# Kernel tuning notes

Hardware: AMD Instinct MI355X
Metric: run time of the kernel (lower is better)

Reference implementation:

```python
import jax, jax.numpy as jnp
import numpy as np

D_MODEL = 1024
D_INNER = 2048   # expand_factor * d_model
D_STATE = 16
D_CONV = 4
DT_RANK = 64     # ceil(d_model / 16)
EPS = 1e-5


def setup_inputs() -> dict:
    key = jax.random.key(0)
    ks = jax.random.split(key, 10)
    B, L = 2, 1024
    w = lambda k, shape, s: (jax.random.normal(k, shape, jnp.float32) * s)
    A = jnp.tile(jnp.arange(1, D_STATE + 1, dtype=jnp.float32), (D_INNER, 1))
    return {
        "hidden_states": jax.random.normal(ks[0], (B, L, D_MODEL), jnp.float32),
        "norm_w": jnp.ones((D_MODEL,), jnp.float32),
        "norm_b": jnp.zeros((D_MODEL,), jnp.float32),
        "in_proj_w": w(ks[1], (D_MODEL, 2 * D_INNER), 0.02),
        "conv_w": w(ks[2], (D_INNER, D_CONV), 0.2),
        "conv_b": jnp.zeros((D_INNER,), jnp.float32),
        "x_proj_w": w(ks[3], (D_INNER, DT_RANK + 2 * D_STATE), 0.02),
        "dt_proj_w": w(ks[4], (DT_RANK, D_INNER), 0.1),
        "dt_proj_b": w(ks[5], (D_INNER,), 0.1),
        "A_log": jnp.log(A),
        "D_param": jnp.ones((D_INNER,), jnp.float32),
        "out_proj_w": w(ks[6], (D_INNER, D_MODEL), 0.02),
    }


def _causal_depthwise_conv(x, conv_w, conv_b):
    # x: [B, L, d_inner] -> causal depthwise conv, kernel size D_CONV
    B, L, C = x.shape
    xt = jnp.transpose(x, (0, 2, 1))                 # [B, C, L]
    xt = jnp.pad(xt, ((0, 0), (0, 0), (D_CONV - 1, 0)))  # left pad == torch pad+truncate
    k = conv_w[:, None, :]                            # [C, 1, K] (OIH, groups=C)
    y = jax.lax.conv_general_dilated(
        xt, k, window_strides=(1,), padding="VALID",
        dimension_numbers=("NCH", "OIH", "NCH"), feature_group_count=C)
    y = y + conv_b[None, :, None]
    return jnp.transpose(y, (0, 2, 1))                # [B, L, C]


def _selective_scan(u, delta, A, Bm, Cm, D_param):
    # u, delta: [B, L, d_inner]; A: [d_inner, d_state]; Bm, Cm: [B, L, d_state]
    dA = jnp.exp(delta[..., None] * A[None, None])            # [B,L,d,n]
    dBu = delta[..., None] * Bm[:, :, None, :] * u[..., None]  # [B,L,d,n]
    h0 = jnp.zeros((u.shape[0], u.shape[2], A.shape[1]), u.dtype)

    def step(h, inp):
        dA_t, dBu_t, c_t = inp          # [B,d,n], [B,d,n], [B,n]
        h = dA_t * h + dBu_t
        y = jnp.einsum("bdn,bn->bd", h, c_t)
        return h, y

    xs = (jnp.moveaxis(dA, 1, 0), jnp.moveaxis(dBu, 1, 0), jnp.moveaxis(Cm, 1, 0))
    _, ys = jax.lax.scan(step, h0, xs)   # ys: [L, B, d]
    y = jnp.moveaxis(ys, 0, 1)           # [B, L, d]
    return y + u * D_param[None, None]


def reference(hidden_states, norm_w, norm_b, in_proj_w, conv_w, conv_b,
              x_proj_w, dt_proj_w, dt_proj_b, A_log, D_param, out_proj_w):
    h = hidden_states
    mu = jnp.mean(h, axis=-1, keepdims=True)
    var = jnp.mean(jnp.square(h - mu), axis=-1, keepdims=True)
    h = (h - mu) * jax.lax.rsqrt(var + EPS) * norm_w + norm_b

    xz = h @ in_proj_w                       # [B,L,2*d_inner]
    x, z = jnp.split(xz, 2, axis=-1)
    x = _causal_depthwise_conv(x, conv_w, conv_b)
    x = jax.nn.silu(x)

    A = -jnp.exp(A_log)                      # [d_inner, d_state]
    xp = x @ x_proj_w                        # [B,L,dt_rank+2*d_state]
    dt_r = xp[..., :DT_RANK]
    Bm = xp[..., DT_RANK:DT_RANK + D_STATE]
    Cm = xp[..., DT_RANK + D_STATE:]
    delta = jax.nn.softplus(dt_r @ dt_proj_w + dt_proj_b)  # [B,L,d_inner]

    y = _selective_scan(x, delta, A, Bm, Cm, D_param)
    y = y * jax.nn.silu(z)
    return y @ out_proj_w
```

## Files before the change

### kernel.cpp

```cpp
#include <hip/hip_runtime.h>
#include <hip/hip_bf16.h>

#define D_MODEL 1024
#define D_INNER 2048
#define D_STATE 16
#define DT_RANK 64
#define NB 2
#define LSEQ 1024
#define NROWS (NB * LSEQ)
#define XPN 96
#define NC 32
#define CL 32

typedef __attribute__((ext_vector_type(8))) short bf16x8;
typedef __attribute__((ext_vector_type(4))) float f32x4;

__device__ __forceinline__ unsigned short f2bf(float x) {
    __hip_bfloat16 h = __float2bfloat16(x);
    return *reinterpret_cast<unsigned short*>(&h);
}
__device__ __forceinline__ float bf2f(unsigned short u) {
    unsigned int v = ((unsigned int)u) << 16;
    float f;
    __builtin_memcpy(&f, &v, 4);
    return f;
}
__device__ __forceinline__ unsigned short f2h(float x) {
    _Float16 h = (_Float16)x;
    unsigned short u;
    __builtin_memcpy(&u, &h, 2);
    return u;
}
__device__ __forceinline__ float h2f(unsigned short u) {
    _Float16 h;
    __builtin_memcpy(&h, &u, 2);
    return (float)h;
}

__global__ __launch_bounds__(256) void ln_kernel(const float* __restrict__ x,
                                                 const float* __restrict__ w,
                                                 const float* __restrict__ bnorm,
                                                 unsigned short* __restrict__ outb) {
    int row = blockIdx.x;
    const float4* xr = (const float4*)(x + (size_t)row * D_MODEL);
    float4 v = xr[threadIdx.x];
    float s = v.x + v.y + v.z + v.w;
    float sq = v.x * v.x + v.y * v.y + v.z * v.z + v.w * v.w;
#pragma unroll
    for (int off = 32; off > 0; off >>= 1) {
        s += __shfl_down(s, off);
        sq += __shfl_down(sq, off);
    }
    __shared__ float ws[4], wq[4];
    __shared__ float smu, srstd;
    int wave = threadIdx.x >> 6;
    if ((threadIdx.x & 63) == 0) { ws[wave] = s; wq[wave] = sq; }
    __syncthreads();
    if (threadIdx.x == 0) {
        float ts = ws[0] + ws[1] + ws[2] + ws[3];
        float tq = wq[0] + wq[1] + wq[2] + wq[3];
        float mu = ts * (1.f / D_MODEL);
        float var = tq * (1.f / D_MODEL) - mu * mu;
        smu = mu;
        srstd = rsqrtf(var + 1e-5f);
    }
    __syncthreads();
    float mu = smu, rstd = srstd;
    float4 wv = ((const float4*)w)[threadIdx.x];
    float4 bv = ((const float4*)bnorm)[threadIdx.x];
    ushort4 pk;
    pk.x = f2bf((v.x - mu) * rstd * wv.x + bv.x);
    pk.y = f2bf((v.y - mu) * rstd * wv.y + bv.y);
    pk.z = f2bf((v.z - mu) * rstd * wv.z + bv.z);
    pk.w = f2bf((v.w - mu) * rstd * wv.w + bv.w);
    *(ushort4*)(outb + (size_t)row * D_MODEL + threadIdx.x * 4) = pk;
}

__global__ __launch_bounds__(256) void wcast_all(const float* __restrict__ W0, unsigned short* __restrict__ D0,
                                                 const float* __restrict__ W1, unsigned short* __restrict__ D1,
                                                 const float* __restrict__ W2, unsigned short* __restrict__ D2,
                                                 const float* __restrict__ W3, unsigned short* __restrict__ D3) {
    int bid = blockIdx.x;
    const float* W;
    unsigned short* Dst;
    int K, Nreal, bx, by;
    if (bid < 4096) { W = W0; Dst = D0; K = 1024; Nreal = 4096; bx = bid & 127; by = bid >> 7; }
    else if (bid < 4352) { int j = bid - 4096; W = W1; Dst = D1; K = 2048; Nreal = 96; bx = j & 3; by = j >> 2; }
    else if (bid < 6400) { int j = bid - 4352; W = W2; Dst = D2; K = 2048; Nreal = 1024; bx = j & 31; by = j >> 5; }
    else { int j = bid - 6400; W = W3; Dst = D3; K = 64; Nreal = 2048; bx = j & 63; by = j >> 6; }
    __shared__ float t[32][33];
    int tn = bx * 32, tk = by * 32;
    for (int e = threadIdx.x; e < 1024; e += 256) {
        int r = e >> 5, c = e & 31;
        int n = tn + c;
        t[r][c] = (n < Nreal) ? W[(size_t)(tk + r) * Nreal + n] : 0.f;
    }
    __syncthreads();
    for (int e = threadIdx.x; e < 1024; e += 256) {
        int r = e >> 5, c = e & 31;
        Dst[(size_t)(tn + r) * K + tk + c] = f2bf(t[c][r]);
    }
}

template <int EPI>
__global__ __launch_bounds__(256) void gemm_bf16(const unsigned short* __restrict__ A,
                                                 const unsigned short* __restrict__ Bt,
                                                 const float* __restrict__ bias,
                                                 float* __restrict__ C,
                                                 void* __restrict__ C2,
                                                 int M, int K, int ldc, int Nreal) {
    __shared__ unsigned short As[128 * 32];
    __shared__ unsigned short Bs[128 * 32];
    int nwg = gridDim.x * gridDim.y;
    int orig = blockIdx.y * gridDim.x + blockIdx.x;
    int q = nwg >> 3, r = nwg & 7;
    int xcd = orig & 7, idx = orig >> 3;
    int newid = (xcd < r ? xcd * (q + 1) : r * (q + 1) + (xcd - r) * q) + idx;
    int bx = newid % gridDim.x, by = newid / gridDim.x;

    int tid = threadIdx.x;
    int lane = tid & 63;
    int wave = tid >> 6;
    int wr = (wave >> 1) * 64, wc = (wave & 1) * 64;
    int bm = by * 128, bn = bx * 128;
    int kchunk = K / gridDim.z;
    int kbeg = blockIdx.z * kchunk;

    f32x4 acc[4][4];
#pragma unroll
    for (int i = 0; i < 4; ++i)
#pragma unroll
        for (int j = 0; j < 4; ++j) acc[i][j] = (f32x4){0.f, 0.f, 0.f, 0.f};

    int r0 = tid >> 2;
    int c0 = (tid & 3) * 8;
    const unsigned short* a0 = A + (size_t)(bm + r0) * K + c0;
    const unsigned short* a1 = A + (size_t)(bm + 64 + r0) * K + c0;
    const unsigned short* b0 = Bt + (size_t)(bn + r0) * K + c0;
    const unsigned short* b1 = Bt + (size_t)(bn + 64 + r0) * K + c0;
    unsigned short* asw0 = As + (size_t)(tid & ~63) * 8;
    unsigned short* asw1 = As + 2048 + (size_t)(tid & ~63) * 8;
    unsigned short* bsw0 = Bs + (size_t)(tid & ~63) * 8;
    unsigned short* bsw1 = Bs + 2048 + (size_t)(tid & ~63) * 8;

    int ar = lane & 15;
    int ko = (lane >> 4) * 8;

    for (int k0 = kbeg; k0 < kbeg + kchunk; k0 += 32) {
        __syncthreads();
        __builtin_amdgcn_global_load_lds((const __attribute__((address_space(1))) void*)(a0 + k0),
                                         (__attribute__((address_space(3))) void*)asw0, 16, 0, 0);
        __builtin_amdgcn_global_load_lds((const __attribute__((address_space(1))) void*)(a1 + k0),
                                         (__attribute__((address_space(3))) void*)asw1, 16, 0, 0);
        __builtin_amdgcn_global_load_lds((const __attribute__((address_space(1))) void*)(b0 + k0),
                                         (__attribute__((address_space(3))) void*)bsw0, 16, 0, 0);
        __builtin_amdgcn_global_load_lds((const __attribute__((address_space(1))) void*)(b1 + k0),
                                         (__attribute__((address_space(3))) void*)bsw1, 16, 0, 0);
        __syncthreads();
        bf16x8 af[4], bfr[4];
#pragma unroll
        for (int i = 0; i < 4; ++i)
            af[i] = *(const bf16x8*)&As[(size_t)(wr + i * 16 + ar) * 32 + ko];
#pragma unroll
        for (int j = 0; j < 4; ++j)
            bfr[j] = *(const bf16x8*)&Bs[(size_t)(wc + j * 16 + ar) * 32 + ko];
#pragma unroll
        for (int i = 0; i < 4; ++i)
#pragma unroll
            for (int j = 0; j < 4; ++j)
                acc[i][j] = __builtin_amdgcn_mfma_f32_16x16x32_bf16(af[i], bfr[j], acc[i][j], 0, 0, 0);
    }

    int crow0 = bm + wr + (lane >> 4) * 4;
    int ccol0 = bn + wc + (lane & 15);
    size_t zoff = (size_t)blockIdx.z * (size_t)M * ldc;
#pragma unroll
    for (int i = 0; i < 4; ++i)
#pragma unroll
        for (int j = 0; j < 4; ++j) {
            int col = ccol0 + j * 16;
            if (EPI == 0) {
                if (col < Nreal) {
                    float* cp = C + zoff + (size_t)(crow0 + i * 16) * ldc + col;
#pragma unroll
                    for (int rr = 0; rr < 4; ++rr) cp[(size_t)rr * ldc] = acc[i][j][rr];
                }
            } else if (EPI == 2) {
                unsigned short* cx = (unsigned short*)C;
                unsigned short* cz = (unsigned short*)C2;
                if (col < 2048) {
#pragma unroll
                    for (int rr = 0; rr < 4; ++rr)
                        cx[(size_t)(crow0 + i * 16 + rr) * 2048 + col] = f2bf(acc[i][j][rr]);
                } else {
#pragma unroll
                    for (int rr = 0; rr < 4; ++rr)
                        cz[(size_t)(crow0 + i * 16 + rr) * 2048 + (col - 2048)] = f2bf(acc[i][j][rr]);
                }
            } else if (EPI == 3) {
                unsigned short* cp = (unsigned short*)C2 + zoff + (size_t)(crow0 + i * 16) * ldc + col;
#pragma unroll
                for (int rr = 0; rr < 4; ++rr) cp[(size_t)rr * ldc] = f2h(acc[i][j][rr]);
            } else {
                float bv = bias[col];
                unsigned short* cp = (unsigned short*)C2 + (size_t)(crow0 + i * 16) * ldc + col;
#pragma unroll
                for (int rr = 0; rr < 4; ++rr) {
                    float v = acc[i][j][rr] + bv;
                    v = (v > 20.f) ? v : log1pf(__expf(v));
                    cp[(size_t)rr * ldc] = f2bf(v);
                }
            }
        }
}

__global__ __launch_bounds__(256) void reduce_xp(const float* __restrict__ part,
                                                 float* __restrict__ xp,
                                                 unsigned short* __restrict__ dtr) {
    int t = blockIdx.x * 256 + threadIdx.x;
    float s = 0.f;
#pragma unroll
    for (int k = 0; k < 16; ++k) s += part[(size_t)k * ((size_t)NROWS * XPN) + t];
    xp[t] = s;
    int row = t / 96, col = t - row * 96;
    if (col < 64) dtr[(size_t)row * 64 + col] = f2bf(s);
}

__global__ __launch_bounds__(256) void reduce_out(const unsigned short* __restrict__ part,
                                                  float* __restrict__ out) {
    int t = blockIdx.x * 256 + threadIdx.x;
    const size_t stride = (size_t)NROWS * D_MODEL;
    ushort4 p0 = ((const ushort4*)part)[t];
    ushort4 p1 = ((const ushort4*)(part + stride))[t];
    ushort4 p2 = ((const ushort4*)(part + 2 * stride))[t];
    ushort4 p3 = ((const ushort4*)(part + 3 * stride))[t];
    float4 o;
    o.x = h2f(p0.x) + h2f(p1.x) + h2f(p2.x) + h2f(p3.x);
    o.y = h2f(p0.y) + h2f(p1.y) + h2f(p2.y) + h2f(p3.y);
    o.z = h2f(p0.z) + h2f(p1.z) + h2f(p2.z) + h2f(p3.z);
    o.w = h2f(p0.w) + h2f(p1.w) + h2f(p2.w) + h2f(p3.w);
    ((float4*)out)[t] = o;
}

__global__ __launch_bounds__(256) void conv_silu_kernel(const unsigned short* __restrict__ xx,
                                                        const float* __restrict__ cw,
                                                        const float* __restrict__ cb,
                                                        unsigned short* __restrict__ outb) {
    int gid = blockIdx.x * 256 + threadIdx.x;
    int d4 = (gid & 511) << 2;
    int bl = gid >> 9;
    int l = bl & (LSEQ - 1);
    const unsigned short* base = xx + (size_t)bl * D_INNER + d4;
    ushort4 zr4 = {0, 0, 0, 0};
    ushort4 X0 = *(const ushort4*)base;
    ushort4 X1 = (l >= 1) ? *(const ushort4*)(base - D_INNER) : zr4;
    ushort4 X2 = (l >= 2) ? *(const ushort4*)(base - 2 * D_INNER) : zr4;
    ushort4 X3 = (l >= 3) ? *(const ushort4*)(base - 3 * D_INNER) : zr4;
    float4 bias = *(const float4*)(cb + d4);
    const float4* wv = (const float4*)(cw + (size_t)d4 * 4);
    float xs0[4] = {bf2f(X0.x), bf2f(X0.y), bf2f(X0.z), bf2f(X0.w)};
    float xs1[4] = {bf2f(X1.x), bf2f(X1.y), bf2f(X1.z), bf2f(X1.w)};
    float xs2[4] = {bf2f(X2.x), bf2f(X2.y), bf2f(X2.z), bf2f(X2.w)};
    float xs3[4] = {bf2f(X3.x), bf2f(X3.y), bf2f(X3.z), bf2f(X3.w)};
    float bs[4] = {bias.x, bias.y, bias.z, bias.w};
    ushort4 ob;
    unsigned short* obp = (unsigned short*)&ob;
#pragma unroll
    for (int e = 0; e < 4; ++e) {
        float4 we = wv[e];
        float acc = bs[e];
        acc = fmaf(we.w, xs0[e], acc);
        acc = fmaf(we.z, xs1[e], acc);
        acc = fmaf(we.y, xs2[e], acc);
        acc = fmaf(we.x, xs3[e], acc);
        obp[e] = f2bf(acc / (1.f + __expf(-acc)));
    }
    *(ushort4*)(outb + (size_t)bl * D_INNER + d4) = ob;
}

__global__ __launch_bounds__(256) void scan_local(const float* __restrict__ xp,
                                                  const unsigned short* __restrict__ delta,
                                                  const unsigned short* __restrict__ ub,
                                                  const float* __restrict__ A_log,
                                                  float* __restrict__ hst,
                                                  float* __restrict__ sdel) {
    int bc = blockIdx.x >> 3;
    int b = bc >> 5, c = bc & (NC - 1);
    int d = (blockIdx.x & 7) * 256 + threadIdx.x;
    int base_r = b * LSEQ + c * CL;
    __shared__ float Bsm[CL * 16];
    for (int e = threadIdx.x; e < CL * 16; e += 256) {
        int l = e >> 4, n = e & 15;
        Bsm[e] = xp[(size_t)(base_r + l) * XPN + DT_RANK + n];
    }
    __syncthreads();
    float Av[16];
    const float4* ap = (const float4*)(A_log + (size_t)d * 16);
#pragma unroll
    for (int qq = 0; qq < 4; ++qq) {
        float4 a = ap[qq];
        Av[4 * qq + 0] = -__expf(a.x); Av[4 * qq + 1] = -__expf(a.y);
        Av[4 * qq + 2] = -__expf(a.z); Av[4 * qq + 3] = -__expf(a.w);
    }
    float h[16] = {};
    float sd = 0.f;
    const unsigned short* dp = delta + (size_t)base_r * D_INNER + d;
    const unsigned short* up = ub + (size_t)base_r * D_INNER + d;
#pragma unroll 4
    for (int l = 0; l < CL; ++l) {
        float dv = bf2f(dp[(size_t)l * D_INNER]);
        float u = bf2f(up[(size_t)l * D_INNER]);
        float du = dv * u;
        sd += dv;
#pragma unroll
        for (int n = 0; n < 16; ++n) {
            float dA = __expf(dv * Av[n]);
            h[n] = fmaf(dA, h[n], du * Bsm[l * 16 + n]);
        }
    }
    size_t hi = ((size_t)(c * NB + b) * D_INNER + d) * 16;
#pragma unroll
    for (int qq = 0; qq < 4; ++qq) {
        float4 v = make_float4(h[4 * qq], h[4 * qq + 1], h[4 * qq + 2], h[4 * qq + 3]);
        *(float4*)(hst + hi + 4 * qq) = v;
    }
    sdel[(size_t)(c * NB + b) * D_INNER + d] = sd;
}

__global__ __launch_bounds__(256) void scan_combine(const float* __restrict__ A_log,
                                                    const float* __restrict__ sdel,
                                                    float* __restrict__ hst) {
    int t = blockIdx.x * 256 + threadIdx.x;
    int n = t & 15, d = (t >> 4) & (D_INNER - 1), b = t >> 15;
    float Avn = -__expf(A_log[(size_t)d * 16 + n]);
    float h = 0.f;
#pragma unroll 4
    for (int c = 0; c < NC; ++c) {
        size_t base = (size_t)(c * NB + b) * D_INNER + d;
        float* hp = hst + base * 16 + n;
        float S = sdel[base];
        float tmp = *hp;
        *hp = h;
        h = fmaf(__expf(Avn * S), h, tmp);
    }
}

__global__ __launch_bounds__(256) void scan_final(const float* __restrict__ xp,
                                                  const unsigned short* __restrict__ delta,
                                                  const unsigned short* __restrict__ ub,
                                                  const unsigned short* __restrict__ zb,
                                                  const float* __restrict__ hst,
                                                  const float* __restrict__ A_log,
                                                  const float* __restrict__ Dp,
                                                  unsigned short* __restrict__ yb) {
    int bc = blockIdx.x >> 3;
    int b = bc >> 5, c = bc & (NC - 1);
    int d = (blockIdx.x & 7) * 256 + threadIdx.x;
    int base_r = b * LSEQ + c * CL;
    __shared__ float Bsm[CL * 16], Csm[CL * 16];
    for (int e = threadIdx.x; e < CL * 16; e += 256) {
        int l = e >> 4, n = e & 15;
        Bsm[e] = xp[(size_t)(base_r + l) * XPN + DT_RANK + n];
        Csm[e] = xp[(size_t)(base_r + l) * XPN + DT_RANK + 16 + n];
    }
    __syncthreads();
    float Av[16];
    const float4* ap = (const float4*)(A_log + (size_t)d * 16);
#pragma unroll
    for (int qq = 0; qq < 4; ++qq) {
        float4 a = ap[qq];
        Av[4 * qq + 0] = -__expf(a.x); Av[4 * qq + 1] = -__expf(a.y);
        Av[4 * qq + 2] = -__expf(a.z); Av[4 * qq + 3] = -__expf(a.w);
    }
    float h[16];
    size_t hi = ((size_t)(c * NB + b) * D_INNER + d) * 16;
#pragma unroll
    for (int qq = 0; qq < 4; ++qq) {
        float4 v = *(const float4*)(hst + hi + 4 * qq);
        h[4 * qq] = v.x; h[4 * qq + 1] = v.y; h[4 * qq + 2] = v.z; h[4 * qq + 3] = v.w;
    }
    float Dv = Dp[d];
    const unsigned short* dp = delta + (size_t)base_r * D_INNER + d;
    const unsigned short* up = ub + (size_t)base_r * D_INNER + d;
    const unsigned short* zp = zb + (size_t)base_r * D_INNER + d;
#pragma unroll 4
    for (int l = 0; l < CL; ++l) {
        float dv = bf2f(dp[(size_t)l * D_INNER]);
        float u = bf2f(up[(size_t)l * D_INNER]);
        float du = dv * u;
        float acc = 0.f;
#pragma unroll
        for (int n = 0; n < 16; ++n) {
            float dA = __expf(dv * Av[n]);
            h[n] = fmaf(dA, h[n], du * Bsm[l * 16 + n]);
            acc = fmaf(h[n], Csm[l * 16 + n], acc);
        }
        float yv = fmaf(u, Dv, acc);
        float zv = bf2f(zp[(size_t)l * D_INNER]);
        float sz = zv / (1.f + __expf(-zv));
        yb[(size_t)(base_r + l) * D_INNER + d] = f2bf(yv * sz);
    }
}

extern "C" void kernel_launch(void* const* d_in, const int* in_sizes, int n_in,
                              void* d_out, int out_size, void* d_ws, size_t ws_size,
                              hipStream_t stream) {
    const float* hidden = (const float*)d_in[0];
    const float* norm_w = (const float*)d_in[1];
    const float* norm_b = (const float*)d_in[2];
    const float* in_proj_w = (const float*)d_in[3];
    const float* conv_w = (const float*)d_in[4];
    const float* conv_b = (const float*)d_in[5];
    const float* x_proj_w = (const float*)d_in[6];
    const float* dt_proj_w = (const float*)d_in[7];
    const float* dt_proj_b = (const float*)d_in[8];
    const float* A_log = (const float*)d_in[9];
    const float* D_param = (const float*)d_in[10];
    const float* out_proj_w = (const float*)d_in[11];
    float* out = (float*)d_out;

    float* wsf = (float*)d_ws;
    unsigned short* hbufb = (unsigned short*)wsf;
    float* xpbuf = wsf;
    float* sdelbuf = wsf + 196608;
    unsigned short* xb = (unsigned short*)(wsf + 1048576);
    float* hst = wsf + 1048576;
    unsigned short* zb = (unsigned short*)(wsf + 3145728);
    unsigned short* ub = (unsigned short*)(wsf + 5242880);
    unsigned short* yb = ub;
    unsigned short* wAt = (unsigned short*)(wsf + 7340032);
    float* xpart = wsf + 7340032;
    unsigned short* opart = (unsigned short*)(wsf + 7340032);
    unsigned short* wXt = (unsigned short*)(wsf + 10485760);
    unsigned short* wDt = (unsigned short*)(wsf + 10616832);
    unsigned short* dtrb = (unsigned short*)(wsf + 10682368);
    unsigned short* deltab = (unsigned short*)(wsf + 11665408);
    unsigned short* wOt = (unsigned short*)(wsf + 13762560);

    wcast_all<<<6528, 256, 0, stream>>>(in_proj_w, wAt, x_proj_w, wXt, out_proj_w, wOt,
                                        dt_proj_w, wDt);

    ln_kernel<<<NROWS, 256, 0, stream>>>(hidden, norm_w, norm_b, hbufb);

    gemm_bf16<2><<<dim3(4096 / 128, NROWS / 128, 1), 256, 0, stream>>>(
        hbufb, wAt, nullptr, (float*)xb, zb, NROWS, 1024, 2048, 4096);

    conv_silu_kernel<<<(NROWS * D_INNER) / 1024, 256, 0, stream>>>(xb, conv_w, conv_b, ub);

    gemm_bf16<0><<<dim3(1, NROWS / 128, 16), 256, 0, stream>>>(
        ub, wXt, nullptr, xpart, nullptr, NROWS, 2048, XPN, XPN);

    reduce_xp<<<(NROWS * XPN) / 256, 256, 0, stream>>>(xpart, xpbuf, dtrb);

    gemm_bf16<4><<<dim3(D_INNER / 128, NROWS / 128, 1), 256, 0, stream>>>(
        dtrb, wDt, dt_proj_b, nullptr, deltab, NROWS, 64, D_INNER, D_INNER);

    scan_local<<<NB * NC * (D_INNER / 256), 256, 0, stream>>>(
        xpbuf, deltab, ub, A_log, hst, sdelbuf);
    scan_combine<<<(NB * D_INNER * D_STATE) / 256, 256, 0, stream>>>(
        A_log, sdelbuf, hst);
    scan_final<<<NB * NC * (D_INNER / 256), 256, 0, stream>>>(
        xpbuf, deltab, ub, zb, hst, A_log, D_param, yb);

    gemm_bf16<3><<<dim3(1024 / 128, NROWS / 128, 4), 256, 0, stream>>>(
        yb, wOt, nullptr, nullptr, opart, NROWS, 2048, 1024, 1024);

    reduce_out<<<(NROWS * D_MODEL / 4) / 256, 256, 0, stream>>>(opart, out);
}
```

Measured before the change: 181.1 us.

## Double GEMM K-tile with XOR-swizzled LDS and fuse layernorm into weight cast

The bf16 MFMA GEMM now stages 64-wide K tiles per iteration instead of 32. It uses an XOR swizzle on the LDS layout to avoid bank conflicts, which halves the number of barrier-synchronised load phases. Layernorm is merged into the weight-cast kernel as extra blocks, removing one launch and letting both run concurrently. LDS per block doubles, which may reduce occupancy.

```diff
diff --git a/kernel.cpp b/kernel.cpp
--- a/kernel.cpp
+++ b/kernel.cpp
@@ -37,50 +37,49 @@
     return (float)h;
 }
 
-__global__ __launch_bounds__(256) void ln_kernel(const float* __restrict__ x,
-                                                 const float* __restrict__ w,
-                                                 const float* __restrict__ bnorm,
-                                                 unsigned short* __restrict__ outb) {
-    int row = blockIdx.x;
-    const float4* xr = (const float4*)(x + (size_t)row * D_MODEL);
-    float4 v = xr[threadIdx.x];
-    float s = v.x + v.y + v.z + v.w;
-    float sq = v.x * v.x + v.y * v.y + v.z * v.z + v.w * v.w;
-#pragma unroll
-    for (int off = 32; off > 0; off >>= 1) {
-        s += __shfl_down(s, off);
-        sq += __shfl_down(sq, off);
-    }
-    __shared__ float ws[4], wq[4];
-    __shared__ float smu, srstd;
-    int wave = threadIdx.x >> 6;
-    if ((threadIdx.x & 63) == 0) { ws[wave] = s; wq[wave] = sq; }
-    __syncthreads();
-    if (threadIdx.x == 0) {
-        float ts = ws[0] + ws[1] + ws[2] + ws[3];
-        float tq = wq[0] + wq[1] + wq[2] + wq[3];
-        float mu = ts * (1.f / D_MODEL);
-        float var = tq * (1.f / D_MODEL) - mu * mu;
-        smu = mu;
-        srstd = rsqrtf(var + 1e-5f);
-    }
-    __syncthreads();
-    float mu = smu, rstd = srstd;
-    float4 wv = ((const float4*)w)[threadIdx.x];
-    float4 bv = ((const float4*)bnorm)[threadIdx.x];
-    ushort4 pk;
-    pk.x = f2bf((v.x - mu) * rstd * wv.x + bv.x);
-    pk.y = f2bf((v.y - mu) * rstd * wv.y + bv.y);
-    pk.z = f2bf((v.z - mu) * rstd * wv.z + bv.z);
-    pk.w = f2bf((v.w - mu) * rstd * wv.w + bv.w);
-    *(ushort4*)(outb + (size_t)row * D_MODEL + threadIdx.x * 4) = pk;
-}
-
-__global__ __launch_bounds__(256) void wcast_all(const float* __restrict__ W0, unsigned short* __restrict__ D0,
-                                                 const float* __restrict__ W1, unsigned short* __restrict__ D1,
-                                                 const float* __restrict__ W2, unsigned short* __restrict__ D2,
-                                                 const float* __restrict__ W3, unsigned short* __restrict__ D3) {
+__global__ __launch_bounds__(256) void wcast_ln(const float* __restrict__ W0, unsigned short* __restrict__ D0,
+                                                const float* __restrict__ W1, unsigned short* __restrict__ D1,
+                                                const float* __restrict__ W2, unsigned short* __restrict__ D2,
+                                                const float* __restrict__ W3, unsigned short* __restrict__ D3,
+                                                const float* __restrict__ hx, const float* __restrict__ nw,
+                                                const float* __restrict__ nb, unsigned short* __restrict__ lnout) {
     int bid = blockIdx.x;
+    if (bid >= 6528) {
+        int row = bid - 6528;
+        const float4* xr = (const float4*)(hx + (size_t)row * D_MODEL);
+        float4 v = xr[threadIdx.x];
+        float s = v.x + v.y + v.z + v.w;
+        float sq = v.x * v.x + v.y * v.y + v.z * v.z + v.w * v.w;
+#pragma unroll
+        for (int off = 32; off > 0; off >>= 1) {
+            s += __shfl_down(s, off);
+            sq += __shfl_down(sq, off);
+        }
+        __shared__ float ws[4], wq[4];
+        __shared__ float smu, srstd;
+        int wave = threadIdx.x >> 6;
+        if ((threadIdx.x & 63) == 0) { ws[wave] = s; wq[wave] = sq; }
+        __syncthreads();
+        if (threadIdx.x == 0) {
+            float ts = ws[0] + ws[1] + ws[2] + ws[3];
+            float tq = wq[0] + wq[1] + wq[2] + wq[3];
+            float mu = ts * (1.f / D_MODEL);
+            float var = tq * (1.f / D_MODEL) - mu * mu;
+            smu = mu;
+            srstd = rsqrtf(var + 1e-5f);
+        }
+        __syncthreads();
+        float mu = smu, rstd = srstd;
+        float4 wv = ((const float4*)nw)[threadIdx.x];
+        float4 bv = ((const float4*)nb)[threadIdx.x];
+        ushort4 pk;
+        pk.x = f2bf((v.x - mu) * rstd * wv.x + bv.x);
+        pk.y = f2bf((v.y - mu) * rstd * wv.y + bv.y);
+        pk.z = f2bf((v.z - mu) * rstd * wv.z + bv.z);
+        pk.w = f2bf((v.w - mu) * rstd * wv.w + bv.w);
+        *(ushort4*)(lnout + (size_t)row * D_MODEL + threadIdx.x * 4) = pk;
+        return;
+    }
     const float* W;
     unsigned short* Dst;
     int K, Nreal, bx, by;
@@ -109,8 +108,8 @@
                                                  float* __restrict__ C,
                                                  void* __restrict__ C2,
                                                  int M, int K, int ldc, int Nreal) {
-    __shared__ unsigned short As[128 * 32];
-    __shared__ unsigned short Bs[128 * 32];
+    __shared__ unsigned short As[128 * 64];
+    __shared__ unsigned short Bs[128 * 64];
     int nwg = gridDim.x * gridDim.y;
     int orig = blockIdx.y * gridDim.x + blockIdx.x;
     int q = nwg >> 3, r = nwg & 7;
@@ -132,43 +131,51 @@
 #pragma unroll
         for (int j = 0; j < 4; ++j) acc[i][j] = (f32x4){0.f, 0.f, 0.f, 0.f};
 
-    int r0 = tid >> 2;
-    int c0 = (tid & 3) * 8;
-    const unsigned short* a0 = A + (size_t)(bm + r0) * K + c0;
-    const unsigned short* a1 = A + (size_t)(bm + 64 + r0) * K + c0;
-    const unsigned short* b0 = Bt + (size_t)(bn + r0) * K + c0;
-    const unsigned short* b1 = Bt + (size_t)(bn + 64 + r0) * K + c0;
-    unsigned short* asw0 = As + (size_t)(tid & ~63) * 8;
-    unsigned short* asw1 = As + 2048 + (size_t)(tid & ~63) * 8;
-    unsigned short* bsw0 = Bs + (size_t)(tid & ~63) * 8;
-    unsigned short* bsw1 = Bs + 2048 + (size_t)(tid & ~63) * 8;
-
     int ar = lane & 15;
-    int ko = (lane >> 4) * 8;
-
-    for (int k0 = kbeg; k0 < kbeg + kchunk; k0 += 32) {
+    int kq = lane >> 4;
+
+    for (int k0 = kbeg; k0 < kbeg + kchunk; k0 += 64) {
         __syncthreads();
-        __builtin_amdgcn_global_load_lds((const __attribute__((address_space(1))) void*)(a0 + k0),
-                                         (__attribute__((address_space(3))) void*)asw0, 16, 0, 0);
-        __builtin_amdgcn_global_load_lds((const __attribute__((address_space(1))) void*)(a1 + k0),
-                                         (__attribute__((address_space(3))) void*)asw1, 16, 0, 0);
-        __builtin_amdgcn_global_load_lds((const __attribute__((address_space(1))) void*)(b0 + k0),
-                                         (__attribute__((address_space(3))) void*)bsw0, 16, 0, 0);
-        __builtin_amdgcn_global_load_lds((const __attribute__((address_space(1))) void*)(b1 + k0),
-                                         (__attribute__((address_space(3))) void*)bsw1, 16, 0, 0);
+#pragma unroll
+        for (int s = 0; s < 4; ++s) {
+            int seg = s * 256 + tid;
+            int row = seg >> 3, p = seg & 7;
+            int c = p ^ (row & 7);
+            __builtin_amdgcn_global_load_lds(
+                (const __attribute__((address_space(1))) void*)(A + (size_t)(bm + row) * K + k0 + c * 8),
+                (__attribute__((address_space(3))) void*)(As + seg * 8), 16, 0, 0);
+        }
+#pragma unroll
+        for (int s = 0; s < 4; ++s) {
+            int seg = s * 256 + tid;
+            int row = seg >> 3, p = seg & 7;
+            int c = p ^ (row & 7);
+            __builtin_amdgcn_global_load_lds(
+                (const __attribute__((address_space(1))) void*)(Bt + (size_t)(bn + row) * K + k0 + c * 8),
+                (__attribute__((address_space(3))) void*)(Bs + seg * 8), 16, 0, 0);
+        }
         __syncthreads();
-        bf16x8 af[4], bfr[4];
-#pragma unroll
-        for (int i = 0; i < 4; ++i)
-            af[i] = *(const bf16x8*)&As[(size_t)(wr + i * 16 + ar) * 32 + ko];
-#pragma unroll
-        for (int j = 0; j < 4; ++j)
-            bfr[j] = *(const bf16x8*)&Bs[(size_t)(wc + j * 16 + ar) * 32 + ko];
-#pragma unroll
-        for (int i = 0; i < 4; ++i)
-#pragma unroll
-            for (int j = 0; j < 4; ++j)
-                acc[i][j] = __builtin_amdgcn_mfma_f32_16x16x32_bf16(af[i], bfr[j], acc[i][j], 0, 0, 0);
+#pragma unroll
+        for (int kk = 0; kk < 2; ++kk) {
+            bf16x8 af[4], bfr[4];
+#pragma unroll
+            for (int i = 0; i < 4; ++i) {
+                int row = wr + i * 16 + ar;
+                int pos = ((kk << 2) | kq) ^ (row & 7);
+                af[i] = *(const bf16x8*)&As[(size_t)row * 64 + pos * 8];
+            }
+#pragma unroll
+            for (int j = 0; j < 4; ++j) {
+                int row = wc + j * 16 + ar;
+                int pos = ((kk << 2) | kq) ^ (row & 7);
+                bfr[j] = *(const bf16x8*)&Bs[(size_t)row * 64 + pos * 8];
+            }
+#pragma unroll
+            for (int i = 0; i < 4; ++i)
+#pragma unroll
+                for (int j = 0; j < 4; ++j)
+                    acc[i][j] = __builtin_amdgcn_mfma_f32_16x16x32_bf16(af[i], bfr[j], acc[i][j], 0, 0, 0);
+        }
     }
 
     int crow0 = bm + wr + (lane >> 4) * 4;
@@ -437,10 +444,8 @@
     unsigned short* deltab = (unsigned short*)(wsf + 11665408);
     unsigned short* wOt = (unsigned short*)(wsf + 13762560);
 
-    wcast_all<<<6528, 256, 0, stream>>>(in_proj_w, wAt, x_proj_w, wXt, out_proj_w, wOt,
-                                        dt_proj_w, wDt);
-
-    ln_kernel<<<NROWS, 256, 0, stream>>>(hidden, norm_w, norm_b, hbufb);
+    wcast_ln<<<6528 + NROWS, 256, 0, stream>>>(in_proj_w, wAt, x_proj_w, wXt, out_proj_w, wOt,
+                                               dt_proj_w, wDt, hidden, norm_w, norm_b, hbufb);
 
     gemm_bf16<2><<<dim3(4096 / 128, NROWS / 128, 1), 256, 0, stream>>>(
         hbufb, wAt, nullptr, (float*)xb, zb, NROWS, 1024, 2048, 4096);
```

New measurement: 168.0 us. 1.08x faster.
